# Kernel optimization log

Measured on AMD Instinct MI355X. Metric: run time of the kernel, lower is better.

The kernel has to match this reference:

```python
import jax, jax.numpy as jnp
import numpy as np

N = 20000   # nodes per branch
E = 320000  # edges per branch
B = 64      # graphs in batch
DT = 768    # text in_dim
DP = 128    # prop in_dim
H = 256     # hid_dim
O = 128     # out_dim
EPS = 1e-5
SLOPE = 0.01
NUM_REL = 2


def _init_conv(key, din, dout):
    k1, k2 = jax.random.split(key)
    s = 1.0 / np.sqrt(din)
    w_rel = jax.random.uniform(k1, (NUM_REL, din, dout), minval=-s, maxval=s, dtype=jnp.float32)
    w_root = jax.random.uniform(k2, (din, dout), minval=-s, maxval=s, dtype=jnp.float32)
    bias = jnp.zeros((dout,), jnp.float32)
    return w_rel, w_root, bias


def setup_inputs() -> dict:
    key = jax.random.key(0)
    ks = jax.random.split(key, 16)
    inp = {}
    inp["x_t"] = jax.random.normal(ks[0], (N, DT), jnp.float32)
    inp["x_p"] = jax.random.normal(ks[1], (N, DP), jnp.float32)
    inp["edge_index_t"] = jax.random.randint(ks[2], (2, E), 0, N)
    inp["edge_type_t"] = jax.random.randint(ks[3], (E,), 0, NUM_REL)
    inp["x_t_batch"] = jnp.sort(jax.random.randint(ks[4], (N,), 0, B))
    inp["edge_index_p"] = jax.random.randint(ks[5], (2, E), 0, N)
    inp["edge_type_p"] = jax.random.randint(ks[6], (E,), 0, NUM_REL)
    inp["x_p_batch"] = jnp.sort(jax.random.randint(ks[7], (N,), 0, B))
    inp["w_t1_rel"], inp["w_t1_root"], inp["b_t1"] = _init_conv(ks[8], DT, H)
    inp["w_t2_rel"], inp["w_t2_root"], inp["b_t2"] = _init_conv(ks[9], H, O)
    inp["w_p1_rel"], inp["w_p1_root"], inp["b_p1"] = _init_conv(ks[10], DP, H)
    inp["w_p2_rel"], inp["w_p2_root"], inp["b_p2"] = _init_conv(ks[11], H, O)
    inp["g_t1"] = jnp.ones((H,), jnp.float32); inp["be_t1"] = jnp.zeros((H,), jnp.float32)
    inp["g_t2"] = jnp.ones((O,), jnp.float32); inp["be_t2"] = jnp.zeros((O,), jnp.float32)
    inp["g_p1"] = jnp.ones((H,), jnp.float32); inp["be_p1"] = jnp.zeros((H,), jnp.float32)
    inp["g_p2"] = jnp.ones((O,), jnp.float32); inp["be_p2"] = jnp.zeros((O,), jnp.float32)
    return inp


def rgcn_conv(x, edge_index, edge_type, w_rel, w_root, bias):
    # PyG RGCNConv: per-relation mean aggregation of W_r x_j, plus root + bias
    src, dst = edge_index[0], edge_index[1]
    out = x @ w_root + bias
    for r in range(NUM_REL):
        h = x @ w_rel[r]                                   # [N, dout]
        mask = (edge_type == r)
        msg = jnp.where(mask[:, None], h[src], 0.0)        # [E, dout]
        s = jax.ops.segment_sum(msg, dst, num_segments=x.shape[0])
        cnt = jax.ops.segment_sum(mask.astype(x.dtype), dst, num_segments=x.shape[0])
        out = out + s / jnp.maximum(cnt, 1.0)[:, None]
    return out


def batchnorm(x, gamma, beta):
    mu = x.mean(0)
    var = x.var(0)  # biased, matching torch normalization
    return (x - mu) * jax.lax.rsqrt(var + EPS) * gamma + beta


def leaky_relu(x):
    return jnp.where(x >= 0, x, SLOPE * x)


def scatter_mean_pool(x, batch, num_graphs):
    s = jax.ops.segment_sum(x, batch, num_segments=num_graphs)
    cnt = jax.ops.segment_sum(jnp.ones((x.shape[0],), x.dtype), batch, num_segments=num_graphs)
    return s / jnp.maximum(cnt, 1.0)[:, None]


def reference(x_t, x_p,
              w_t1_rel, w_t1_root, b_t1, w_t2_rel, w_t2_root, b_t2,
              w_p1_rel, w_p1_root, b_p1, w_p2_rel, w_p2_root, b_p2,
              g_t1, be_t1, g_t2, be_t2, g_p1, be_p1, g_p2, be_p2,
              edge_index_t, edge_type_t, x_t_batch,
              edge_index_p, edge_type_p, x_p_batch):
    h = rgcn_conv(x_t, edge_index_t, edge_type_t, w_t1_rel, w_t1_root, b_t1)
    h = leaky_relu(batchnorm(h, g_t1, be_t1))
    h = rgcn_conv(h, edge_index_t, edge_type_t, w_t2_rel, w_t2_root, b_t2)
    h = leaky_relu(batchnorm(h, g_t2, be_t2))
    out_t = scatter_mean_pool(h, x_t_batch, B)

    h = rgcn_conv(x_p, edge_index_p, edge_type_p, w_p1_rel, w_p1_root, b_p1)
    h = leaky_relu(batchnorm(h, g_p1, be_p1))
    h = rgcn_conv(h, edge_index_p, edge_type_p, w_p2_rel, w_p2_root, b_p2)
    h = leaky_relu(batchnorm(h, g_p2, be_p2))
    out_p = scatter_mean_pool(h, x_p_batch, B)
    return (out_t, out_p)
```

## Files before the change

### kernel.cpp

```cpp
#include <hip/hip_runtime.h>

#define NN 20000
#define NE 320000
#define NB 64
#define BNG 128

typedef __attribute__((ext_vector_type(4))) float f32x4;
typedef __attribute__((ext_vector_type(8))) __bf16 bf16x8;

static __device__ __forceinline__ ushort f2bf(float f) {
    uint u = __builtin_bit_cast(uint, f);
    uint r = (u + 0x7fffu + ((u >> 16) & 1u)) >> 16;
    return (ushort)r;
}
static __device__ __forceinline__ float bf2f(ushort u) {
    return __builtin_bit_cast(float, (uint)u << 16);
}

#define GLD_LDS16(g, l)                                                                     \
    __builtin_amdgcn_global_load_lds((__attribute__((address_space(1))) void*)(g),          \
                                     (__attribute__((address_space(3))) void*)(l), 16, 0, 0)


__global__ __launch_bounds__(256) void k_countpos(const int* __restrict__ ei_t, const int* __restrict__ ei_p,
                                                  int* __restrict__ deg, int* __restrict__ posArr) {
    int e = blockIdx.x * 256 + threadIdx.x;
    if (e >= 2 * NE) return;
    int br = e >= NE;
    int el = e - br * NE;
    const int* ei = br ? ei_p : ei_t;
    int dst = ei[NE + el];
    posArr[e] = atomicAdd(&deg[br * NN + dst], 1);
}

__global__ __launch_bounds__(256) void k_scan_local(const int* __restrict__ deg, int* __restrict__ off,
                                                    int* __restrict__ csum, int n) {
    __shared__ int sh[256];
    int base = blockIdx.x * 256, tid = threadIdx.x;
    int v = (base + tid < n) ? deg[base + tid] : 0;
    sh[tid] = v; __syncthreads();
    for (int o = 1; o < 256; o <<= 1) {
        int t = (tid >= o) ? sh[tid - o] : 0;
        __syncthreads();
        sh[tid] += t;
        __syncthreads();
    }
    if (base + tid < n) off[base + tid] = sh[tid] - v;
    if (tid == 255) csum[blockIdx.x] = sh[255];
}

__global__ void k_scan_csum(int* __restrict__ csum, int* __restrict__ offN, int nc) {
    __shared__ int sh[256];
    int tid = threadIdx.x;
    int v = (tid < nc) ? csum[tid] : 0;
    sh[tid] = v; __syncthreads();
    for (int o = 1; o < 256; o <<= 1) {
        int t = (tid >= o) ? sh[tid - o] : 0;
        __syncthreads();
        sh[tid] += t;
        __syncthreads();
    }
    if (tid < nc) csum[tid] = sh[tid] - v;
    if (tid == 255) offN[0] = sh[255];
}

__global__ __launch_bounds__(256) void k_scan_add(int* __restrict__ off, const int* __restrict__ csum, int n) {
    int i = blockIdx.x * 256 + threadIdx.x;
    if (i < n) off[i] += csum[blockIdx.x];
}

__global__ __launch_bounds__(256) void k_fillpos(const int* __restrict__ ei_t, const int* __restrict__ et_t,
                                                 const int* __restrict__ ei_p, const int* __restrict__ et_p,
                                                 const int* __restrict__ off, const int* __restrict__ posArr,
                                                 int* __restrict__ adj) {
    int e = blockIdx.x * 256 + threadIdx.x;
    if (e >= 2 * NE) return;
    int br = e >= NE;
    int el = e - br * NE;
    const int* ei = br ? ei_p : ei_t;
    const int* et = br ? et_p : et_t;
    int src = ei[el], dst = ei[NE + el], r = et[el];
    int g = br * NN + dst;
    adj[off[g] + posArr[e]] = src | (r << 28);
}


__global__ __launch_bounds__(256) void k_cast_x2(const float* __restrict__ xt, const float* __restrict__ xp,
                                                 ushort* __restrict__ ot, ushort* __restrict__ op,
                                                 int n4t, int n4p) {
    int i = blockIdx.x * 256 + threadIdx.x;
    const float* in; ushort* out; int j;
    if (i < n4t) { in = xt; out = ot; j = i; }
    else { j = i - n4t; if (j >= n4p) return; in = xp; out = op; }
    float4 v = *(const float4*)&in[(size_t)j * 4];
    ushort4 o;
    o.x = f2bf(v.x); o.y = f2bf(v.y); o.z = f2bf(v.z); o.w = f2bf(v.w);
    *(ushort4*)&out[(size_t)j * 4] = o;
}

struct WtJob { const float* root; const float* rel; ushort* dst; int K; int C; };

__global__ __launch_bounds__(256) void k_cast_wt_all(WtJob j0, WtJob j1, WtJob j2, WtJob j3,
                                                     int c1, int c2, int c3) {
    __shared__ float tile[32][33];
    int bid = blockIdx.x;
    WtJob j; int lt;
    if (bid < c1) { j = j0; lt = bid; }
    else if (bid < c2) { j = j1; lt = bid - c1; }
    else if (bid < c3) { j = j2; lt = bid - c2; }
    else { j = j3; lt = bid - c3; }
    int nx = j.K >> 5, ny = j.C >> 5;
    int mat = lt / (nx * ny);
    int r2 = lt - mat * (nx * ny);
    int kx = r2 % nx, cy = r2 / nx;
    int KC = j.K * j.C;
    const float* W = (mat == 0) ? j.root : j.rel + (size_t)(mat - 1) * KC;
    int k0 = kx * 32, c0 = cy * 32;
    int tx = threadIdx.x & 31, ty = threadIdx.x >> 5;
#pragma unroll
    for (int i = 0; i < 4; i++)
        tile[ty + i * 8][tx] = W[(size_t)(k0 + ty + i * 8) * j.C + c0 + tx];
    __syncthreads();
#pragma unroll
    for (int i = 0; i < 4; i++)
        j.dst[(size_t)mat * KC + (size_t)(c0 + ty + i * 8) * j.K + k0 + tx] = f2bf(tile[tx][ty + i * 8]);
}


struct GemmJob { const ushort* A; const ushort* Wt; const float* bias;
                 ushort* root; ushort* h0; ushort* h1; int K; };

__global__ __launch_bounds__(256, 3) void k_gemm_mfma(GemmJob j0, GemmJob j1, int M, int C, int NBR) {
    __shared__ ushort smem[20480];

    int nx = C >> 6;
    int perY = nx * NBR;
    int nwg = gridDim.x;
    int orig = blockIdx.x;
    int q = nwg >> 3, r = nwg & 7;
    int xcd = orig & 7, pos = orig >> 3;
    int wgid = (xcd < r) ? (xcd * (q + 1) + pos) : (r * (q + 1) + (xcd - r) * q + pos);
    int y = wgid / perY, rem = wgid - y * perY;
    int br = rem / nx, x = rem - br * nx;
    GemmJob j = br ? j1 : j0;
    int K = j.K;

    int tid = threadIdx.x;
    int lane = tid & 63, wave = tid >> 6;
    int wr = wave >> 1, wc = wave & 1;
    int rowTile = y * 128, colTile = x * 64;

    f32x4 acc[3][4][2] = {};

    for (int k0 = 0; k0 < K; k0 += 64) {
        __syncthreads();
#pragma unroll
        for (int i = 0; i < 4; i++) {
            int id = i * 256 + tid;
            int rr = id >> 3, ck = id & 7;
            int garow = rowTile + rr;
            if (garow >= M) garow = M - 1;
            GLD_LDS16(j.A + (size_t)garow * K + k0 + ck * 8, &smem[id * 8]);
        }
#pragma unroll
        for (int z = 0; z < 3; z++) {
            const ushort* Bz = j.Wt + (size_t)z * C * K;
#pragma unroll
            for (int i = 0; i < 2; i++) {
                int id = i * 256 + tid;
                int rr = id >> 3, ck = id & 7;
                GLD_LDS16(Bz + (size_t)(colTile + rr) * K + k0 + ck * 8,
                          &smem[8192 + z * 4096 + id * 8]);
            }
        }
        __syncthreads();
#pragma unroll
        for (int kk = 0; kk < 2; kk++) {
            int kb = kk * 32 + (lane >> 4) * 8;
            bf16x8 af[4];
#pragma unroll
            for (int mi = 0; mi < 4; mi++)
                af[mi] = *(const bf16x8*)&smem[(wr * 64 + mi * 16 + (lane & 15)) * 64 + kb];
#pragma unroll
            for (int z = 0; z < 3; z++) {
                bf16x8 bfr[2];
#pragma unroll
                for (int ni = 0; ni < 2; ni++)
                    bfr[ni] = *(const bf16x8*)&smem[8192 + z * 4096 +
                                                    (wc * 32 + ni * 16 + (lane & 15)) * 64 + kb];
#pragma unroll
                for (int mi = 0; mi < 4; mi++)
#pragma unroll
                    for (int ni = 0; ni < 2; ni++)
                        acc[z][mi][ni] =
                            __builtin_amdgcn_mfma_f32_16x16x32_bf16(af[mi], bfr[ni], acc[z][mi][ni], 0, 0, 0);
            }
        }
    }

    int lc = lane & 15, lr4 = (lane >> 4) * 4;
#pragma unroll
    for (int z = 0; z < 3; z++) {
        ushort* H = (z == 0) ? j.root : (z == 1 ? j.h0 : j.h1);
        __syncthreads();
#pragma unroll
        for (int ni = 0; ni < 2; ni++) {
            int cl = wc * 32 + ni * 16 + lc;
            float bj = (z == 0) ? j.bias[colTile + cl] : 0.f;
#pragma unroll
            for (int mi = 0; mi < 4; mi++)
#pragma unroll
                for (int jj = 0; jj < 4; jj++) {
                    int rloc = wr * 64 + mi * 16 + lr4 + jj;
                    int chunk = (cl >> 3) ^ (rloc & 7);
                    smem[rloc * 64 + (chunk << 3) + (cl & 7)] = f2bf(acc[z][mi][ni][jj] + bj);
                }
        }
        __syncthreads();
#pragma unroll
        for (int it = 0; it < 4; it++) {
            int cid = it * 256 + tid;
            int rloc = cid >> 3, cc = cid & 7;
            int grow = rowTile + rloc;
            if (grow < M) {
                int4 v = *(const int4*)&smem[rloc * 64 + ((cc ^ (rloc & 7)) << 3)];
                *(int4*)&H[(size_t)grow * C + colTile + cc * 8] = v;
            }
        }
    }
}


__global__ __launch_bounds__(256) void k_agg256(const int* __restrict__ off, const int* __restrict__ adj,
                                                const ushort* __restrict__ h0t, const ushort* __restrict__ h1t,
                                                ushort* __restrict__ asumt,
                                                const ushort* __restrict__ h0p, const ushort* __restrict__ h1p,
                                                ushort* __restrict__ asump, int perBr) {
    __shared__ float4 shA[2][64];
    __shared__ float4 shB[2][64];
    __shared__ int shc[2][2];
    int br = blockIdx.x >= perBr;
    int bb = blockIdx.x - br * perBr;
    const int* offb = off + br * NN;
    const ushort* h0 = br ? h0p : h0t;
    const ushort* h1 = br ? h1p : h1t;
    ushort* asum = br ? asump : asumt;
    int wave = threadIdx.x >> 6, lane = threadIdx.x & 63;
    int nb = wave >> 1, w = wave & 1;
    int node = bb * 2 + nb;
    int s = offb[node], e = offb[node + 1];
    int len = e - s;
    int mid = s + ((len + 1) >> 1);
    int i0 = w ? mid : s;
    int i1 = w ? e : mid;
    float4 a0 = make_float4(0.f, 0.f, 0.f, 0.f);
    float4 a1 = make_float4(0.f, 0.f, 0.f, 0.f);
    float4 b0 = make_float4(0.f, 0.f, 0.f, 0.f);
    float4 b1 = make_float4(0.f, 0.f, 0.f, 0.f);
    int c0 = 0, c1 = 0;
    int i = i0;
    for (; i + 1 < i1; i += 2) {
        int v0 = adj[i], v1 = adj[i + 1];
        int s0 = v0 & 0x0FFFFFFF, r0 = v0 >> 28;
        int s1 = v1 & 0x0FFFFFFF, r1 = v1 >> 28;
        const ushort* hp0 = r0 ? h1 : h0;
        const ushort* hp1 = r1 ? h1 : h0;
        ushort4 x0 = *(const ushort4*)&hp0[(size_t)s0 * 256 + lane * 4];
        ushort4 x1 = *(const ushort4*)&hp1[(size_t)s1 * 256 + lane * 4];
        if (r0) { a1.x += bf2f(x0.x); a1.y += bf2f(x0.y); a1.z += bf2f(x0.z); a1.w += bf2f(x0.w); c1++; }
        else    { a0.x += bf2f(x0.x); a0.y += bf2f(x0.y); a0.z += bf2f(x0.z); a0.w += bf2f(x0.w); c0++; }
        if (r1) { b1.x += bf2f(x1.x); b1.y += bf2f(x1.y); b1.z += bf2f(x1.z); b1.w += bf2f(x1.w); c1++; }
        else    { b0.x += bf2f(x1.x); b0.y += bf2f(x1.y); b0.z += bf2f(x1.z); b0.w += bf2f(x1.w); c0++; }
    }
    if (i < i1) {
        int v0 = adj[i];
        int s0 = v0 & 0x0FFFFFFF, r0 = v0 >> 28;
        const ushort* hp0 = r0 ? h1 : h0;
        ushort4 x0 = *(const ushort4*)&hp0[(size_t)s0 * 256 + lane * 4];
        if (r0) { a1.x += bf2f(x0.x); a1.y += bf2f(x0.y); a1.z += bf2f(x0.z); a1.w += bf2f(x0.w); c1++; }
        else    { a0.x += bf2f(x0.x); a0.y += bf2f(x0.y); a0.z += bf2f(x0.z); a0.w += bf2f(x0.w); c0++; }
    }
    float4 s0v = make_float4(a0.x + b0.x, a0.y + b0.y, a0.z + b0.z, a0.w + b0.w);
    float4 s1v = make_float4(a1.x + b1.x, a1.y + b1.y, a1.z + b1.z, a1.w + b1.w);
    if (w) {
        shA[nb][lane] = s0v; shB[nb][lane] = s1v;
        if (lane == 0) { shc[nb][0] = c0; shc[nb][1] = c1; }
    }
    __syncthreads();
    if (!w) {
        float4 t0 = shA[nb][lane], t1 = shB[nb][lane];
        c0 += shc[nb][0]; c1 += shc[nb][1];
        float w0 = 1.0f / (float)(c0 > 0 ? c0 : 1);
        float w1 = 1.0f / (float)(c1 > 0 ? c1 : 1);
        ushort4 o;
        o.x = f2bf((s0v.x + t0.x) * w0 + (s1v.x + t1.x) * w1);
        o.y = f2bf((s0v.y + t0.y) * w0 + (s1v.y + t1.y) * w1);
        o.z = f2bf((s0v.z + t0.z) * w0 + (s1v.z + t1.z) * w1);
        o.w = f2bf((s0v.w + t0.w) * w0 + (s1v.w + t1.w) * w1);
        *(ushort4*)&asum[(size_t)node * 256 + lane * 4] = o;
    }
}

__global__ __launch_bounds__(256) void k_agg128(const int* __restrict__ offAll, const int* __restrict__ adj,
                                                const ushort* __restrict__ h0t, const ushort* __restrict__ h1t,
                                                ushort* __restrict__ asumt,
                                                const ushort* __restrict__ h0p, const ushort* __restrict__ h1p,
                                                ushort* __restrict__ asump) {
    int half = gridDim.x >> 1;
    int br = blockIdx.x >= half;
    int bb = blockIdx.x - br * half;
    int wave = threadIdx.x >> 6, lane = threadIdx.x & 63;
    int node = bb * 4 + wave;
    const int* off = offAll + br * NN;
    const ushort* h0 = br ? h0p : h0t;
    const ushort* h1 = br ? h1p : h1t;
    ushort* asum = br ? asump : asumt;
    int s = off[node], e = off[node + 1];
    int l32 = lane & 31, ep = lane >> 5;
    float4 a0 = make_float4(0.f, 0.f, 0.f, 0.f);
    float4 a1 = make_float4(0.f, 0.f, 0.f, 0.f);
    float4 b0 = make_float4(0.f, 0.f, 0.f, 0.f);
    float4 b1 = make_float4(0.f, 0.f, 0.f, 0.f);
    int c0 = 0, c1 = 0;
    int i = s + ep;
    for (; i + 2 < e; i += 4) {
        int v0 = adj[i], v1 = adj[i + 2];
        int s0 = v0 & 0x0FFFFFFF, r0 = v0 >> 28;
        int s1 = v1 & 0x0FFFFFFF, r1 = v1 >> 28;
        const ushort* hp0 = r0 ? h1 : h0;
        const ushort* hp1 = r1 ? h1 : h0;
        ushort4 x0 = *(const ushort4*)&hp0[(size_t)s0 * 128 + l32 * 4];
        ushort4 x1 = *(const ushort4*)&hp1[(size_t)s1 * 128 + l32 * 4];
        if (r0) { a1.x += bf2f(x0.x); a1.y += bf2f(x0.y); a1.z += bf2f(x0.z); a1.w += bf2f(x0.w); c1++; }
        else    { a0.x += bf2f(x0.x); a0.y += bf2f(x0.y); a0.z += bf2f(x0.z); a0.w += bf2f(x0.w); c0++; }
        if (r1) { b1.x += bf2f(x1.x); b1.y += bf2f(x1.y); b1.z += bf2f(x1.z); b1.w += bf2f(x1.w); c1++; }
        else    { b0.x += bf2f(x1.x); b0.y += bf2f(x1.y); b0.z += bf2f(x1.z); b0.w += bf2f(x1.w); c0++; }
    }
    if (i < e) {
        int v0 = adj[i];
        int s0 = v0 & 0x0FFFFFFF, r0 = v0 >> 28;
        const ushort* hp0 = r0 ? h1 : h0;
        ushort4 x0 = *(const ushort4*)&hp0[(size_t)s0 * 128 + l32 * 4];
        if (r0) { a1.x += bf2f(x0.x); a1.y += bf2f(x0.y); a1.z += bf2f(x0.z); a1.w += bf2f(x0.w); c1++; }
        else    { a0.x += bf2f(x0.x); a0.y += bf2f(x0.y); a0.z += bf2f(x0.z); a0.w += bf2f(x0.w); c0++; }
    }
    float sx0 = a0.x + b0.x, sy0 = a0.y + b0.y, sz0 = a0.z + b0.z, sw0 = a0.w + b0.w;
    float sx1 = a1.x + b1.x, sy1 = a1.y + b1.y, sz1 = a1.z + b1.z, sw1 = a1.w + b1.w;
    sx0 += __shfl_xor(sx0, 32); sy0 += __shfl_xor(sy0, 32);
    sz0 += __shfl_xor(sz0, 32); sw0 += __shfl_xor(sw0, 32);
    sx1 += __shfl_xor(sx1, 32); sy1 += __shfl_xor(sy1, 32);
    sz1 += __shfl_xor(sz1, 32); sw1 += __shfl_xor(sw1, 32);
    c0 += __shfl_xor(c0, 32); c1 += __shfl_xor(c1, 32);
    if (ep == 0) {
        float w0 = 1.0f / (float)(c0 > 0 ? c0 : 1);
        float w1 = 1.0f / (float)(c1 > 0 ? c1 : 1);
        ushort4 o;
        o.x = f2bf(sx0 * w0 + sx1 * w1);
        o.y = f2bf(sy0 * w0 + sy1 * w1);
        o.z = f2bf(sz0 * w0 + sz1 * w1);
        o.w = f2bf(sw0 * w0 + sw1 * w1);
        *(ushort4*)&asum[(size_t)node * 128 + l32 * 4] = o;
    }
}


__global__ __launch_bounds__(256) void k_bnstats(const ushort* __restrict__ r0, const ushort* __restrict__ s0,
                                                 const ushort* __restrict__ r1, const ushort* __restrict__ s1,
                                                 float* __restrict__ part, int C, int M) {
    int br = blockIdx.y;
    const ushort* root = br ? r1 : r0;
    const ushort* asum = br ? s1 : s0;
    float* P = part + (size_t)br * 2 * C * BNG;
    int tid = threadIdx.x;
    int half = C >> 1;
    int groups = 256 / half;
    int col2 = tid & (half - 1);
    int rg = tid / half;
    float sx = 0.f, sy = 0.f, qx = 0.f, qy = 0.f;
    for (int row = blockIdx.x * groups + rg; row < M; row += BNG * groups) {
        uint rv = *(const uint*)&root[(size_t)row * C + col2 * 2];
        uint av = *(const uint*)&asum[(size_t)row * C + col2 * 2];
        float v0 = bf2f((ushort)(rv & 0xffff)) + bf2f((ushort)(av & 0xffff));
        float v1 = bf2f((ushort)(rv >> 16)) + bf2f((ushort)(av >> 16));
        sx += v0; qx += v0 * v0;
        sy += v1; qy += v1 * v1;
    }
    __shared__ float4 sh[256];
    sh[tid] = make_float4(sx, sy, qx, qy);
    __syncthreads();
    if (tid < half) {
        float4 a = sh[tid];
        for (int g = 1; g < groups; g++) {
            float4 b = sh[tid + g * half];
            a.x += b.x; a.y += b.y; a.z += b.z; a.w += b.w;
        }
        int c0 = tid * 2;
        P[(size_t)c0 * BNG + blockIdx.x] = a.x;
        P[(size_t)(c0 + 1) * BNG + blockIdx.x] = a.y;
        P[(size_t)(C + c0) * BNG + blockIdx.x] = a.z;
        P[(size_t)(C + c0 + 1) * BNG + blockIdx.x] = a.w;
    }
}

__global__ __launch_bounds__(256) void k_bnreduce(const float* __restrict__ part,
                                                  const float* __restrict__ g0, const float* __restrict__ be0,
                                                  const float* __restrict__ g1, const float* __restrict__ be1,
                                                  float* __restrict__ ss, int C, float invM) {
    int br = blockIdx.y;
    const float* P = part + (size_t)br * 2 * C * BNG;
    const float* g = br ? g1 : g0;
    const float* be = br ? be1 : be0;
    float* S = ss + br * 2 * C;
    int wv = threadIdx.x >> 6, lane = threadIdx.x & 63;
    int c = blockIdx.x * 4 + wv;
    if (c >= C) return;
    float s = P[(size_t)c * BNG + lane] + P[(size_t)c * BNG + 64 + lane];
    float s2 = P[(size_t)(C + c) * BNG + lane] + P[(size_t)(C + c) * BNG + 64 + lane];
#pragma unroll
    for (int o = 32; o >= 1; o >>= 1) {
        s += __shfl_xor(s, o, 64);
        s2 += __shfl_xor(s2, o, 64);
    }
    if (lane == 0) {
        float mu = s * invM;
        float var = s2 * invM - mu * mu;
        float sc = g[c] * rsqrtf(var + 1e-5f);
        S[c] = sc;
        S[C + c] = be[c] - mu * sc;
    }
}

__global__ __launch_bounds__(256) void k_bnapply(const ushort* __restrict__ r0, const ushort* __restrict__ s0,
                                                 const ushort* __restrict__ r1, const ushort* __restrict__ s1,
                                                 const float* __restrict__ ss, int C, int M,
                                                 ushort* __restrict__ ob0, ushort* __restrict__ ob1) {
    int br = blockIdx.y;
    const ushort* root = br ? r1 : r0;
    const ushort* asum = br ? s1 : s0;
    const float* S = ss + br * 2 * C;
    int i = blockIdx.x * 256 + threadIdx.x;
    int total4 = M * C / 4;
    if (i >= total4) return;
    ushort4 rv = *(const ushort4*)&root[(size_t)i * 4];
    ushort4 av = *(const ushort4*)&asum[(size_t)i * 4];
    int c0 = (i * 4) & (C - 1);
    float y0 = (bf2f(rv.x) + bf2f(av.x)) * S[c0 + 0] + S[C + c0 + 0];
    float y1 = (bf2f(rv.y) + bf2f(av.y)) * S[c0 + 1] + S[C + c0 + 1];
    float y2 = (bf2f(rv.z) + bf2f(av.z)) * S[c0 + 2] + S[C + c0 + 2];
    float y3 = (bf2f(rv.w) + bf2f(av.w)) * S[c0 + 3] + S[C + c0 + 3];
    y0 = y0 >= 0.f ? y0 : 0.01f * y0;
    y1 = y1 >= 0.f ? y1 : 0.01f * y1;
    y2 = y2 >= 0.f ? y2 : 0.01f * y2;
    y3 = y3 >= 0.f ? y3 : 0.01f * y3;
    ushort* ob = br ? ob1 : ob0;
    ushort4 o;
    o.x = f2bf(y0); o.y = f2bf(y1); o.z = f2bf(y2); o.w = f2bf(y3);
    *(ushort4*)&ob[(size_t)i * 4] = o;
}


__global__ __launch_bounds__(512) void k_pool2(const ushort* __restrict__ r2t, const ushort* __restrict__ s2t,
                                               const ushort* __restrict__ r2p, const ushort* __restrict__ s2p,
                                               const int* __restrict__ bt, const int* __restrict__ bp,
                                               const float* __restrict__ ss, float* __restrict__ out) {
    int blk = blockIdx.x;
    int br = blk >> 6, b = blk & 63;
    const ushort* root = br ? r2p : r2t;
    const ushort* asum = br ? s2p : s2t;
    const int* bat = br ? bp : bt;
    const float* S = ss + br * 2 * 128;
    __shared__ int se[2];
    if (threadIdx.x < 2) {
        int val = b + (int)threadIdx.x;
        int lo = 0, hi = NN;
        while (lo < hi) {
            int mid = (lo + hi) >> 1;
            if (bat[mid] < val) lo = mid + 1; else hi = mid;
        }
        se[threadIdx.x] = lo;
    }
    __syncthreads();
    int s = se[0], e = se[1];
    int t2 = threadIdx.x & 63, rg = threadIdx.x >> 6;
    float sc0 = S[t2 * 2], sh0 = S[128 + t2 * 2];
    float sc1 = S[t2 * 2 + 1], sh1 = S[128 + t2 * 2 + 1];
    float ax = 0.f, ay = 0.f;
    for (int r = s + rg; r < e; r += 8) {
        uint rv = *(const uint*)&root[(size_t)r * 128 + t2 * 2];
        uint av = *(const uint*)&asum[(size_t)r * 128 + t2 * 2];
        float v0 = (bf2f((ushort)(rv & 0xffff)) + bf2f((ushort)(av & 0xffff))) * sc0 + sh0;
        float v1 = (bf2f((ushort)(rv >> 16)) + bf2f((ushort)(av >> 16))) * sc1 + sh1;
        v0 = v0 >= 0.f ? v0 : 0.01f * v0;
        v1 = v1 >= 0.f ? v1 : 0.01f * v1;
        ax += v0; ay += v1;
    }
    __shared__ float2 sh[512];
    sh[threadIdx.x] = make_float2(ax, ay);
    __syncthreads();
    if (rg == 0) {
        float2 a = sh[t2];
#pragma unroll
        for (int g = 1; g < 8; g++) {
            float2 v = sh[t2 + g * 64];
            a.x += v.x; a.y += v.y;
        }
        int cnt = e - s;
        float inv = 1.0f / (float)(cnt > 0 ? cnt : 1);
        out[(br * 64 + b) * 128 + t2 * 2] = a.x * inv;
        out[(br * 64 + b) * 128 + t2 * 2 + 1] = a.y * inv;
    }
}


extern "C" void kernel_launch(void* const* d_in, const int* in_sizes, int n_in,
                              void* d_out, int out_size, void* d_ws, size_t ws_size,
                              hipStream_t stream) {
    const float* x_t = (const float*)d_in[0];
    const float* x_p = (const float*)d_in[1];
    const int* ei_t = (const int*)d_in[2];
    const int* et_t = (const int*)d_in[3];
    const int* bat_t = (const int*)d_in[4];
    const int* ei_p = (const int*)d_in[5];
    const int* et_p = (const int*)d_in[6];
    const int* bat_p = (const int*)d_in[7];
    const float* w_t1_rel = (const float*)d_in[8];
    const float* w_t1_root = (const float*)d_in[9];
    const float* b_t1 = (const float*)d_in[10];
    const float* w_t2_rel = (const float*)d_in[11];
    const float* w_t2_root = (const float*)d_in[12];
    const float* b_t2 = (const float*)d_in[13];
    const float* w_p1_rel = (const float*)d_in[14];
    const float* w_p1_root = (const float*)d_in[15];
    const float* b_p1 = (const float*)d_in[16];
    const float* w_p2_rel = (const float*)d_in[17];
    const float* w_p2_root = (const float*)d_in[18];
    const float* b_p2 = (const float*)d_in[19];
    const float* g_t1 = (const float*)d_in[20]; const float* be_t1 = (const float*)d_in[21];
    const float* g_t2 = (const float*)d_in[22]; const float* be_t2 = (const float*)d_in[23];
    const float* g_p1 = (const float*)d_in[24]; const float* be_p1 = (const float*)d_in[25];
    const float* g_p2 = (const float*)d_in[26]; const float* be_p2 = (const float*)d_in[27];

    char* wp = (char*)d_ws;
    auto alloc = [&](size_t b) -> void* {
        void* p = (void*)wp;
        wp += (b + 255) & ~(size_t)255;
        return p;
    };

    const bool MERGED = ws_size >= (size_t)137 * 1000 * 1000;

    dim3 blk(256);
    const int EB2 = (2 * NE) / 256;
    const int SCB2 = (2 * NN + 255) / 256;
    const int nMT = (NN + 127) / 128;

    ushort* xt_bf; ushort* xp_bf;
    ushort *h0t1, *h1t1, *h0p1, *h1p1;
    ushort *root1t, *asum1t, *root1p, *asum1p;
    ushort *a1t, *a1p;
    ushort *root2t, *asum2t, *root2p, *asum2p;
    ushort *h0t2, *h1t2, *h0p2, *h1p2;
    ushort* wtb; int* adj; int* posArr; int* off; int* deg; int* csum;
    float* part; float* ss;

    if (MERGED) {
        xt_bf = (ushort*)alloc((size_t)NN * 768 * 2);
        xp_bf = (ushort*)alloc((size_t)NN * 128 * 2);
        h0t1 = (ushort*)alloc((size_t)NN * 256 * 2);
        h1t1 = (ushort*)alloc((size_t)NN * 256 * 2);
        h0p1 = (ushort*)alloc((size_t)NN * 256 * 2);
        h1p1 = (ushort*)alloc((size_t)NN * 256 * 2);
        root1t = (ushort*)alloc((size_t)NN * 256 * 2);
        asum1t = (ushort*)alloc((size_t)NN * 256 * 2);
        root1p = (ushort*)alloc((size_t)NN * 256 * 2);
        asum1p = (ushort*)alloc((size_t)NN * 256 * 2);
        a1t = (ushort*)alloc((size_t)NN * 256 * 2);
        wtb = (ushort*)alloc((size_t)(3 * 768 * 256 + 3 * 128 * 256 + 2 * 3 * 256 * 128) * 2);
        adj = (int*)alloc((size_t)2 * NE * 4);
        posArr = (int*)alloc((size_t)2 * NE * 4);
        off = (int*)alloc((size_t)(2 * NN + 1) * 4);
        deg = (int*)alloc((size_t)2 * NN * 4);
        csum = (int*)alloc(256 * 4);
        part = (float*)alloc((size_t)2 * 2 * 256 * BNG * 4);
        ss = (float*)alloc(1024 * 4);
        root2t = xt_bf;
        asum2t = root2t + (size_t)NN * 128;
        root2p = asum2t + (size_t)NN * 128;
        asum2p = root2p + (size_t)NN * 128;
        a1p    = asum2p + (size_t)NN * 128;
        h0t2 = h0t1;                       h0p2 = h0t1 + (size_t)NN * 128;
        h1t2 = h1t1;                       h1p2 = h1t1 + (size_t)NN * 128;
    } else {
        xt_bf = (ushort*)alloc((size_t)NN * 768 * 2);
        xp_bf = (ushort*)alloc((size_t)NN * 128 * 2);
        ushort* h0b = (ushort*)alloc((size_t)NN * 256 * 2);
        ushort* h1b = (ushort*)alloc((size_t)NN * 256 * 2);
        ushort* root1 = (ushort*)alloc((size_t)NN * 256 * 2);
        ushort* asum1 = (ushort*)alloc((size_t)NN * 256 * 2);
        a1t = (ushort*)alloc((size_t)NN * 256 * 2);
        wtb = (ushort*)alloc((size_t)(3 * 768 * 256 + 3 * 128 * 256 + 2 * 3 * 256 * 128) * 2);
        adj = (int*)alloc((size_t)2 * NE * 4);
        posArr = (int*)alloc((size_t)2 * NE * 4);
        off = (int*)alloc((size_t)(2 * NN + 1) * 4);
        deg = (int*)alloc((size_t)2 * NN * 4);
        csum = (int*)alloc(256 * 4);
        part = (float*)alloc((size_t)2 * 2 * 256 * BNG * 4);
        ss = (float*)alloc(1024 * 4);
        h0t1 = h0b; h1t1 = h1b; h0p1 = h0b; h1p1 = h1b;
        root1t = root1; asum1t = asum1; root1p = root1; asum1p = asum1;
        root2t = xt_bf;
        asum2t = root2t + (size_t)NN * 128;
        root2p = asum2t + (size_t)NN * 128;
        asum2p = root2p + (size_t)NN * 128;
        a1p    = asum2p + (size_t)NN * 128;
        h0t2 = h0b;                        h0p2 = h0b + (size_t)NN * 128;
        h1t2 = h1b;                        h1p2 = h1b + (size_t)NN * 128;
    }

    hipMemsetAsync(deg, 0, (size_t)2 * NN * 4, stream);
    k_countpos<<<EB2, blk, 0, stream>>>(ei_t, ei_p, deg, posArr);
    k_scan_local<<<SCB2, blk, 0, stream>>>(deg, off, csum, 2 * NN);
    k_scan_csum<<<1, 256, 0, stream>>>(csum, off + 2 * NN, SCB2);
    k_scan_add<<<SCB2, blk, 0, stream>>>(off, csum, 2 * NN);
    k_fillpos<<<EB2, blk, 0, stream>>>(ei_t, et_t, ei_p, et_p, off, posArr, adj);

    int n4t = NN * 768 / 4, n4p = NN * 128 / 4;
    k_cast_x2<<<(n4t + n4p + 255) / 256, blk, 0, stream>>>(x_t, x_p, xt_bf, xp_bf, n4t, n4p);

    ushort* wt_t1 = wtb;
    ushort* wt_p1 = wt_t1 + 3 * 768 * 256;
    ushort* wt_t2 = wt_p1 + 3 * 128 * 256;
    ushort* wt_p2 = wt_t2 + 3 * 256 * 128;
    WtJob j0 = {w_t1_root, w_t1_rel, wt_t1, 768, 256};
    WtJob j1 = {w_p1_root, w_p1_rel, wt_p1, 128, 256};
    WtJob j2 = {w_t2_root, w_t2_rel, wt_t2, 256, 128};
    WtJob j3 = {w_p2_root, w_p2_rel, wt_p2, 256, 128};
    k_cast_wt_all<<<864, blk, 0, stream>>>(j0, j1, j2, j3, 576, 672, 768);

    GemmJob Gt1 = {xt_bf, wt_t1, b_t1, root1t, h0t1, h1t1, 768};
    GemmJob Gp1 = {xp_bf, wt_p1, b_p1, root1p, h0p1, h1p1, 128};

    if (MERGED) {
        k_gemm_mfma<<<nMT * 4 * 2, blk, 0, stream>>>(Gt1, Gp1, NN, 256, 2);
        k_agg256<<<NN, blk, 0, stream>>>(off, adj, h0t1, h1t1, asum1t, h0p1, h1p1, asum1p, NN / 2);
        k_bnstats<<<dim3(BNG, 2), blk, 0, stream>>>(root1t, asum1t, root1p, asum1p, part, 256, NN);
        k_bnreduce<<<dim3(64, 2), blk, 0, stream>>>(part, g_t1, be_t1, g_p1, be_p1, ss, 256, 1.0f / NN);
        k_bnapply<<<dim3((NN * 256 / 4 + 255) / 256, 2), blk, 0, stream>>>(
            root1t, asum1t, root1p, asum1p, ss, 256, NN, a1t, a1p);
    } else {
        k_gemm_mfma<<<nMT * 4, blk, 0, stream>>>(Gt1, Gt1, NN, 256, 1);
        k_agg256<<<NN / 2, blk, 0, stream>>>(off, adj, h0t1, h1t1, asum1t, h0t1, h1t1, asum1t, NN / 2);
        k_bnstats<<<dim3(BNG, 1), blk, 0, stream>>>(root1t, asum1t, root1t, asum1t, part, 256, NN);
        k_bnreduce<<<dim3(64, 1), blk, 0, stream>>>(part, g_t1, be_t1, g_t1, be_t1, ss, 256, 1.0f / NN);
        k_bnapply<<<dim3((NN * 256 / 4 + 255) / 256, 1), blk, 0, stream>>>(
            root1t, asum1t, root1t, asum1t, ss, 256, NN, a1t, a1t);

        k_gemm_mfma<<<nMT * 4, blk, 0, stream>>>(Gp1, Gp1, NN, 256, 1);
        k_agg256<<<NN / 2, blk, 0, stream>>>(off + NN, adj, h0p1, h1p1, asum1p, h0p1, h1p1, asum1p, NN / 2);
        k_bnstats<<<dim3(BNG, 1), blk, 0, stream>>>(root1p, asum1p, root1p, asum1p, part, 256, NN);
        k_bnreduce<<<dim3(64, 1), blk, 0, stream>>>(part, g_p1, be_p1, g_p1, be_p1, ss, 256, 1.0f / NN);
        k_bnapply<<<dim3((NN * 256 / 4 + 255) / 256, 1), blk, 0, stream>>>(
            root1p, asum1p, root1p, asum1p, ss, 256, NN, a1p, a1p);
    }

    GemmJob Gt2 = {a1t, wt_t2, b_t2, root2t, h0t2, h1t2, 256};
    GemmJob Gp2 = {a1p, wt_p2, b_p2, root2p, h0p2, h1p2, 256};
    k_gemm_mfma<<<nMT * 2 * 2, blk, 0, stream>>>(Gt2, Gp2, NN, 128, 2);
    k_agg128<<<2 * (NN / 4), blk, 0, stream>>>(off, adj, h0t2, h1t2, asum2t, h0p2, h1p2, asum2p);
    k_bnstats<<<dim3(BNG, 2), blk, 0, stream>>>(root2t, asum2t, root2p, asum2p, part, 128, NN);
    k_bnreduce<<<dim3(32, 2), blk, 0, stream>>>(part, g_t2, be_t2, g_p2, be_p2, ss, 128, 1.0f / NN);

    k_pool2<<<128, 512, 0, stream>>>(root2t, asum2t, root2p, asum2p, bat_t, bat_p, ss, (float*)d_out);
}
```

Before: 301.4 us.

## Merge prep kernels into one launch and fold adjacency fill into first GEMM

The edge degree counting, the input bf16 cast and the weight transpose-cast now run as block ranges of a single prep kernel instead of three separate launches. The CSR adjacency fill is appended as extra blocks of the first-layer GEMM launch, so it overlaps with GEMM work rather than running as its own kernel. This removes several launches and their serialization gaps. In exchange, the GEMM kernel carries an extra branch, and the XCD remap now uses the GEMM block count rather than the full grid size.

```diff
diff --git a/kernel.cpp b/kernel.cpp
--- a/kernel.cpp
+++ b/kernel.cpp
@@ -21,17 +21,65 @@
     __builtin_amdgcn_global_load_lds((__attribute__((address_space(1))) void*)(g),          \
                                      (__attribute__((address_space(3))) void*)(l), 16, 0, 0)
 
-
-__global__ __launch_bounds__(256) void k_countpos(const int* __restrict__ ei_t, const int* __restrict__ ei_p,
-                                                  int* __restrict__ deg, int* __restrict__ posArr) {
-    int e = blockIdx.x * 256 + threadIdx.x;
-    if (e >= 2 * NE) return;
-    int br = e >= NE;
-    int el = e - br * NE;
-    const int* ei = br ? ei_p : ei_t;
-    int dst = ei[NE + el];
-    posArr[e] = atomicAdd(&deg[br * NN + dst], 1);
-}
+struct WtJob { const float* root; const float* rel; ushort* dst; int K; int C; };
+struct FillArgs { const int* ei_t; const int* et_t; const int* ei_p; const int* et_p;
+                  const int* off; const int* posArr; int* adj; };
+
+
+__global__ __launch_bounds__(256) void k_prep(const int* __restrict__ ei_t, const int* __restrict__ ei_p,
+                                              int* __restrict__ deg, int* __restrict__ posArr,
+                                              const float* __restrict__ xt, const float* __restrict__ xp,
+                                              ushort* __restrict__ ot, ushort* __restrict__ op,
+                                              int n4t, int n4p,
+                                              WtJob j0, WtJob j1, WtJob j2, WtJob j3,
+                                              int c1, int c2, int c3, int nbCount, int nbCast) {
+    __shared__ float tile[32][33];
+    int bid = blockIdx.x;
+    int tid = threadIdx.x;
+    if (bid < nbCount) {
+        int e = bid * 256 + tid;
+        if (e >= 2 * NE) return;
+        int br = e >= NE;
+        int el = e - br * NE;
+        const int* ei = br ? ei_p : ei_t;
+        int dst = ei[NE + el];
+        posArr[e] = atomicAdd(&deg[br * NN + dst], 1);
+        return;
+    }
+    if (bid < nbCount + nbCast) {
+        int i = (bid - nbCount) * 256 + tid;
+        const float* in; ushort* out; int j;
+        if (i < n4t) { in = xt; out = ot; j = i; }
+        else { j = i - n4t; if (j >= n4p) return; in = xp; out = op; }
+        float4 v = *(const float4*)&in[(size_t)j * 4];
+        ushort4 o;
+        o.x = f2bf(v.x); o.y = f2bf(v.y); o.z = f2bf(v.z); o.w = f2bf(v.w);
+        *(ushort4*)&out[(size_t)j * 4] = o;
+        return;
+    }
+    int lt0 = bid - nbCount - nbCast;
+    WtJob j; int lt;
+    if (lt0 < c1) { j = j0; lt = lt0; }
+    else if (lt0 < c2) { j = j1; lt = lt0 - c1; }
+    else if (lt0 < c3) { j = j2; lt = lt0 - c2; }
+    else { j = j3; lt = lt0 - c3; }
+    int nx = j.K >> 5, ny = j.C >> 5;
+    int mat = lt / (nx * ny);
+    int r2 = lt - mat * (nx * ny);
+    int kx = r2 % nx, cy = r2 / nx;
+    int KC = j.K * j.C;
+    const float* W = (mat == 0) ? j.root : j.rel + (size_t)(mat - 1) * KC;
+    int k0 = kx * 32, c0 = cy * 32;
+    int tx = tid & 31, ty = tid >> 5;
+#pragma unroll
+    for (int i = 0; i < 4; i++)
+        tile[ty + i * 8][tx] = W[(size_t)(k0 + ty + i * 8) * j.C + c0 + tx];
+    __syncthreads();
+#pragma unroll
+    for (int i = 0; i < 4; i++)
+        j.dst[(size_t)mat * KC + (size_t)(c0 + ty + i * 8) * j.K + k0 + tx] = f2bf(tile[tx][ty + i * 8]);
+}
+
 
 __global__ __launch_bounds__(256) void k_scan_local(const int* __restrict__ deg, int* __restrict__ off,
                                                     int* __restrict__ csum, int n) {
@@ -69,75 +117,31 @@
     if (i < n) off[i] += csum[blockIdx.x];
 }
 
-__global__ __launch_bounds__(256) void k_fillpos(const int* __restrict__ ei_t, const int* __restrict__ et_t,
-                                                 const int* __restrict__ ei_p, const int* __restrict__ et_p,
-                                                 const int* __restrict__ off, const int* __restrict__ posArr,
-                                                 int* __restrict__ adj) {
-    int e = blockIdx.x * 256 + threadIdx.x;
-    if (e >= 2 * NE) return;
-    int br = e >= NE;
-    int el = e - br * NE;
-    const int* ei = br ? ei_p : ei_t;
-    const int* et = br ? et_p : et_t;
-    int src = ei[el], dst = ei[NE + el], r = et[el];
-    int g = br * NN + dst;
-    adj[off[g] + posArr[e]] = src | (r << 28);
-}
-
-
-__global__ __launch_bounds__(256) void k_cast_x2(const float* __restrict__ xt, const float* __restrict__ xp,
-                                                 ushort* __restrict__ ot, ushort* __restrict__ op,
-                                                 int n4t, int n4p) {
-    int i = blockIdx.x * 256 + threadIdx.x;
-    const float* in; ushort* out; int j;
-    if (i < n4t) { in = xt; out = ot; j = i; }
-    else { j = i - n4t; if (j >= n4p) return; in = xp; out = op; }
-    float4 v = *(const float4*)&in[(size_t)j * 4];
-    ushort4 o;
-    o.x = f2bf(v.x); o.y = f2bf(v.y); o.z = f2bf(v.z); o.w = f2bf(v.w);
-    *(ushort4*)&out[(size_t)j * 4] = o;
-}
-
-struct WtJob { const float* root; const float* rel; ushort* dst; int K; int C; };
-
-__global__ __launch_bounds__(256) void k_cast_wt_all(WtJob j0, WtJob j1, WtJob j2, WtJob j3,
-                                                     int c1, int c2, int c3) {
-    __shared__ float tile[32][33];
-    int bid = blockIdx.x;
-    WtJob j; int lt;
-    if (bid < c1) { j = j0; lt = bid; }
-    else if (bid < c2) { j = j1; lt = bid - c1; }
-    else if (bid < c3) { j = j2; lt = bid - c2; }
-    else { j = j3; lt = bid - c3; }
-    int nx = j.K >> 5, ny = j.C >> 5;
-    int mat = lt / (nx * ny);
-    int r2 = lt - mat * (nx * ny);
-    int kx = r2 % nx, cy = r2 / nx;
-    int KC = j.K * j.C;
-    const float* W = (mat == 0) ? j.root : j.rel + (size_t)(mat - 1) * KC;
-    int k0 = kx * 32, c0 = cy * 32;
-    int tx = threadIdx.x & 31, ty = threadIdx.x >> 5;
-#pragma unroll
-    for (int i = 0; i < 4; i++)
-        tile[ty + i * 8][tx] = W[(size_t)(k0 + ty + i * 8) * j.C + c0 + tx];
-    __syncthreads();
-#pragma unroll
-    for (int i = 0; i < 4; i++)
-        j.dst[(size_t)mat * KC + (size_t)(c0 + ty + i * 8) * j.K + k0 + tx] = f2bf(tile[tx][ty + i * 8]);
-}
-
 
 struct GemmJob { const ushort* A; const ushort* Wt; const float* bias;
                  ushort* root; ushort* h0; ushort* h1; int K; };
 
-__global__ __launch_bounds__(256, 3) void k_gemm_mfma(GemmJob j0, GemmJob j1, int M, int C, int NBR) {
+__global__ __launch_bounds__(256, 3) void k_gemm_fill(GemmJob j0, GemmJob j1, int M, int C, int NBR,
+                                                      int nwgG, FillArgs fa) {
     __shared__ ushort smem[20480];
+
+    if ((int)blockIdx.x >= nwgG) {
+        int e = ((int)blockIdx.x - nwgG) * 256 + threadIdx.x;
+        if (e >= 2 * NE) return;
+        int br = e >= NE;
+        int el = e - br * NE;
+        const int* ei = br ? fa.ei_p : fa.ei_t;
+        const int* et = br ? fa.et_p : fa.et_t;
+        int src = ei[el], dst = ei[NE + el], r = et[el];
+        int g = br * NN + dst;
+        fa.adj[fa.off[g] + fa.posArr[e]] = src | (r << 28);
+        return;
+    }
 
     int nx = C >> 6;
     int perY = nx * NBR;
-    int nwg = gridDim.x;
     int orig = blockIdx.x;
-    int q = nwg >> 3, r = nwg & 7;
+    int q = nwgG >> 3, r = nwgG & 7;
     int xcd = orig & 7, pos = orig >> 3;
     int wgid = (xcd < r) ? (xcd * (q + 1) + pos) : (r * (q + 1) + (xcd - r) * q + pos);
     int y = wgid / perY, rem = wgid - y * perY;
@@ -617,16 +621,6 @@
         h1t2 = h1b;                        h1p2 = h1b + (size_t)NN * 128;
     }
 
-    hipMemsetAsync(deg, 0, (size_t)2 * NN * 4, stream);
-    k_countpos<<<EB2, blk, 0, stream>>>(ei_t, ei_p, deg, posArr);
-    k_scan_local<<<SCB2, blk, 0, stream>>>(deg, off, csum, 2 * NN);
-    k_scan_csum<<<1, 256, 0, stream>>>(csum, off + 2 * NN, SCB2);
-    k_scan_add<<<SCB2, blk, 0, stream>>>(off, csum, 2 * NN);
-    k_fillpos<<<EB2, blk, 0, stream>>>(ei_t, et_t, ei_p, et_p, off, posArr, adj);
-
-    int n4t = NN * 768 / 4, n4p = NN * 128 / 4;
-    k_cast_x2<<<(n4t + n4p + 255) / 256, blk, 0, stream>>>(x_t, x_p, xt_bf, xp_bf, n4t, n4p);
-
     ushort* wt_t1 = wtb;
     ushort* wt_p1 = wt_t1 + 3 * 768 * 256;
     ushort* wt_t2 = wt_p1 + 3 * 128 * 256;
@@ -635,27 +629,40 @@
     WtJob j1 = {w_p1_root, w_p1_rel, wt_p1, 128, 256};
     WtJob j2 = {w_t2_root, w_t2_rel, wt_t2, 256, 128};
     WtJob j3 = {w_p2_root, w_p2_rel, wt_p2, 256, 128};
-    k_cast_wt_all<<<864, blk, 0, stream>>>(j0, j1, j2, j3, 576, 672, 768);
-
+
+    int n4t = NN * 768 / 4, n4p = NN * 128 / 4;
+    int nbCast = (n4t + n4p + 255) / 256;
+
+    hipMemsetAsync(deg, 0, (size_t)2 * NN * 4, stream);
+    k_prep<<<EB2 + nbCast + 864, blk, 0, stream>>>(ei_t, ei_p, deg, posArr,
+                                                   x_t, x_p, xt_bf, xp_bf, n4t, n4p,
+                                                   j0, j1, j2, j3, 576, 672, 768, EB2, nbCast);
+    k_scan_local<<<SCB2, blk, 0, stream>>>(deg, off, csum, 2 * NN);
+    k_scan_csum<<<1, 256, 0, stream>>>(csum, off + 2 * NN, SCB2);
+    k_scan_add<<<SCB2, blk, 0, stream>>>(off, csum, 2 * NN);
+
+    FillArgs fa = {ei_t, et_t, ei_p, et_p, off, posArr, adj};
     GemmJob Gt1 = {xt_bf, wt_t1, b_t1, root1t, h0t1, h1t1, 768};
     GemmJob Gp1 = {xp_bf, wt_p1, b_p1, root1p, h0p1, h1p1, 128};
 
     if (MERGED) {
-        k_gemm_mfma<<<nMT * 4 * 2, blk, 0, stream>>>(Gt1, Gp1, NN, 256, 2);
+        int nwgG = nMT * 4 * 2;
+        k_gemm_fill<<<nwgG + EB2, blk, 0, stream>>>(Gt1, Gp1, NN, 256, 2, nwgG, fa);
         k_agg256<<<NN, blk, 0, stream>>>(off, adj, h0t1, h1t1, asum1t, h0p1, h1p1, asum1p, NN / 2);
         k_bnstats<<<dim3(BNG, 2), blk, 0, stream>>>(root1t, asum1t, root1p, asum1p, part, 256, NN);
         k_bnreduce<<<dim3(64, 2), blk, 0, stream>>>(part, g_t1, be_t1, g_p1, be_p1, ss, 256, 1.0f / NN);
         k_bnapply<<<dim3((NN * 256 / 4 + 255) / 256, 2), blk, 0, stream>>>(
             root1t, asum1t, root1p, asum1p, ss, 256, NN, a1t, a1p);
     } else {
-        k_gemm_mfma<<<nMT * 4, blk, 0, stream>>>(Gt1, Gt1, NN, 256, 1);
+        int nwgG = nMT * 4;
+        k_gemm_fill<<<nwgG + EB2, blk, 0, stream>>>(Gt1, Gt1, NN, 256, 1, nwgG, fa);
         k_agg256<<<NN / 2, blk, 0, stream>>>(off, adj, h0t1, h1t1, asum1t, h0t1, h1t1, asum1t, NN / 2);
         k_bnstats<<<dim3(BNG, 1), blk, 0, stream>>>(root1t, asum1t, root1t, asum1t, part, 256, NN);
         k_bnreduce<<<dim3(64, 1), blk, 0, stream>>>(part, g_t1, be_t1, g_t1, be_t1, ss, 256, 1.0f / NN);
         k_bnapply<<<dim3((NN * 256 / 4 + 255) / 256, 1), blk, 0, stream>>>(
             root1t, asum1t, root1t, asum1t, ss, 256, NN, a1t, a1t);
 
-        k_gemm_mfma<<<nMT * 4, blk, 0, stream>>>(Gp1, Gp1, NN, 256, 1);
+        k_gemm_fill<<<nwgG, blk, 0, stream>>>(Gp1, Gp1, NN, 256, 1, nwgG, fa);
         k_agg256<<<NN / 2, blk, 0, stream>>>(off + NN, adj, h0p1, h1p1, asum1p, h0p1, h1p1, asum1p, NN / 2);
         k_bnstats<<<dim3(BNG, 1), blk, 0, stream>>>(root1p, asum1p, root1p, asum1p, part, 256, NN);
         k_bnreduce<<<dim3(64, 1), blk, 0, stream>>>(part, g_p1, be_p1, g_p1, be_p1, ss, 256, 1.0f / NN);
@@ -665,7 +672,8 @@
 
     GemmJob Gt2 = {a1t, wt_t2, b_t2, root2t, h0t2, h1t2, 256};
     GemmJob Gp2 = {a1p, wt_p2, b_p2, root2p, h0p2, h1p2, 256};
-    k_gemm_mfma<<<nMT * 2 * 2, blk, 0, stream>>>(Gt2, Gp2, NN, 128, 2);
+    int nwg2 = nMT * 2 * 2;
+    k_gemm_fill<<<nwg2, blk, 0, stream>>>(Gt2, Gp2, NN, 128, 2, nwg2, fa);
     k_agg128<<<2 * (NN / 4), blk, 0, stream>>>(off, adj, h0t2, h1t2, asum2t, h0p2, h1p2, asum2p);
     k_bnstats<<<dim3(BNG, 2), blk, 0, stream>>>(root2t, asum2t, root2p, asum2p, part, 128, NN);
     k_bnreduce<<<dim3(32, 2), blk, 0, stream>>>(part, g_t2, be_t2, g_p2, be_p2, ss, 128, 1.0f / NN);
```

After: 287.7 us. -4.6%, faster.
